# Performance work log

Measured on AMD Instinct MI355X. Metric: run time of the kernel, lower is better.

## Reference

```python
import jax, jax.numpy as jnp
import numpy as np

B = 4096
N_DENSE = 13
N_SPARSE = 26
VOCAB = 100000
EMB = 8
CIN_SIZE = [26, 128, 128]


def setup_inputs() -> dict:
    key = jax.random.key(0)
    ks = jax.random.split(key, 24)
    s = 0.05
    dense = jax.random.normal(ks[0], (B, N_DENSE), dtype=jnp.float32)
    sparse = jax.random.randint(ks[1], (B, N_SPARSE), 0, VOCAB).astype(jnp.float32)
    inputs = jnp.concatenate([dense, sparse], axis=1)  # [B, 39]
    emb_tables = jax.random.normal(ks[2], (N_SPARSE, VOCAB, EMB), dtype=jnp.float32) * s
    linear_W = jax.random.normal(ks[3], (39, 1), dtype=jnp.float32) * s
    linear_b = jnp.zeros((1,), dtype=jnp.float32)
    # CIN Conv3d weights: kernel (H_prev, H0, 1) with out_channels H_next -> [H_next, H_prev, H0]
    W_cin0 = jax.random.normal(ks[4], (CIN_SIZE[1], CIN_SIZE[0], CIN_SIZE[0]), dtype=jnp.float32) * s
    b_cin0 = jnp.zeros((CIN_SIZE[1],), dtype=jnp.float32)
    W_cin1 = jax.random.normal(ks[5], (CIN_SIZE[2], CIN_SIZE[1], CIN_SIZE[0]), dtype=jnp.float32) * s
    b_cin1 = jnp.zeros((CIN_SIZE[2],), dtype=jnp.float32)
    cin_lin_W = jax.random.normal(ks[6], (256, 1), dtype=jnp.float32) * s
    cin_lin_b = jnp.zeros((1,), dtype=jnp.float32)
    d_W1 = jax.random.normal(ks[7], (221, 256), dtype=jnp.float32) * s
    d_b1 = jnp.zeros((256,), dtype=jnp.float32)
    d_W2 = jax.random.normal(ks[8], (256, 128), dtype=jnp.float32) * s
    d_b2 = jnp.zeros((128,), dtype=jnp.float32)
    d_W3 = jax.random.normal(ks[9], (128, 64), dtype=jnp.float32) * s
    d_b3 = jnp.zeros((64,), dtype=jnp.float32)
    d_W4 = jax.random.normal(ks[10], (64, 1), dtype=jnp.float32) * s
    d_b4 = jnp.zeros((1,), dtype=jnp.float32)
    return dict(inputs=inputs, emb_tables=emb_tables, linear_W=linear_W, linear_b=linear_b,
                W_cin0=W_cin0, b_cin0=b_cin0, W_cin1=W_cin1, b_cin1=b_cin1,
                cin_lin_W=cin_lin_W, cin_lin_b=cin_lin_b,
                d_W1=d_W1, d_b1=d_b1, d_W2=d_W2, d_b2=d_b2,
                d_W3=d_W3, d_b3=d_b3, d_W4=d_W4, d_b4=d_b4)


def reference(inputs, emb_tables, linear_W, linear_b,
              W_cin0, b_cin0, W_cin1, b_cin1, cin_lin_W, cin_lin_b,
              d_W1, d_b1, d_W2, d_b2, d_W3, d_b3, d_W4, d_b4):
    dense_in = inputs[:, :N_DENSE]                       # [B, 13]
    sparse_idx = inputs[:, N_DENSE:].astype(jnp.int32)   # [B, 26]

    # linear part over the raw inputs
    linear_out = inputs @ linear_W + linear_b            # [B, 1]

    # per-field embedding lookup: tables [F, V, E], idx [B, F] -> emb [B, F, E]
    emb = jax.vmap(lambda t, i: t[i], in_axes=(0, 1), out_axes=1)(emb_tables, sparse_idx)

    # CIN: each layer is an outer product over fields followed by a full-extent
    # Conv3d, i.e. X_{l+1}[b,o,k] = sum_{i,j} X_l[b,i,k] * X_0[b,j,k] * W[o,i,j] + b[o]
    X0 = emb
    Xi = emb
    res = []
    for W, b in ((W_cin0, b_cin0), (W_cin1, b_cin1)):
        Xi = jnp.einsum('bik,bjk,oij->bok', Xi, X0, W) + b[None, :, None]
        res.append(Xi)
    cin_feat = jnp.sum(jnp.concatenate(res, axis=1), axis=-1)  # [B, 256]
    cin_out = jax.nn.relu(cin_feat @ cin_lin_W + cin_lin_b)    # [B, 1]

    # dense MLP over [dense | flattened embeddings]
    h = jnp.concatenate([dense_in, emb.reshape(emb.shape[0], -1)], axis=1)  # [B, 221]
    h = jax.nn.relu(h @ d_W1 + d_b1)
    h = jax.nn.relu(h @ d_W2 + d_b2)
    h = jax.nn.relu(h @ d_W3 + d_b3)
    dense_out = jax.nn.relu(h @ d_W4 + d_b4)                   # [B, 1]

    return jax.nn.sigmoid(linear_out + cin_out + dense_out).reshape(-1)  # [B]
```

## Files before the change

### kernel.cpp

```cpp
#include <hip/hip_runtime.h>
#include <math.h>

#define B     4096
#define ND    13
#define NS    26
#define NF    39
#define VOCAB 100000
#define NP    351
#define NPP   360
#define CHP   45
#define GSTR  28
#define RPB   4
#define XSS   212

#define OFF_GST 0
#define OFF_CST 10080
#define OFF_C2J 10088

__global__ __launch_bounds__(256) void k_pre(const float* __restrict__ W0,
                                             const float* __restrict__ W1,
                                             const float* __restrict__ b0,
                                             const float* __restrict__ b1,
                                             const float* __restrict__ clw,
                                             float* __restrict__ Gst,
                                             float* __restrict__ cst,
                                             float* __restrict__ c2j) {
    int blk = blockIdx.x, tid = threadIdx.x;
    if (blk < 26) {
        int j = blk;
        __shared__ float vh[2][128];
        __shared__ float vj[128];
        __shared__ float c2r[2];
        {
            int i = tid & 127, h = tid >> 7;
            const float* wp = W1 + (long)(h * 64) * 3328 + i * 26 + j;
            float acc = 0.f;
#pragma unroll 8
            for (int o = 0; o < 64; o++) acc += clw[128 + h * 64 + o] * wp[o * 3328];
            vh[h][i] = acc;
        }
        __syncthreads();
        if (tid < 128) {
            float vv = vh[0][tid] + vh[1][tid];
            vj[tid] = vv;
            float c = vv * b0[tid];
            for (int off = 32; off; off >>= 1) c += __shfl_down(c, off, 64);
            if ((tid & 63) == 0) c2r[tid >> 6] = c;
        }
        __syncthreads();
        if (tid == 0) c2j[j] = c2r[0] + c2r[1];
        for (int p = tid; p < NPP; p += 256) {
            float g = 0.f;
            if (p < NP) {
                int l = 0, rem = p;
                while (rem >= NS - l) { rem -= NS - l; l++; }
                int m = l + rem;
                float sym = (l != m) ? 1.f : 0.f;
                const float* wa = W0 + l * 26 + m;
                const float* wb = W0 + m * 26 + l;
#pragma unroll 8
                for (int i = 0; i < 128; i++)
                    g += vj[i] * (wa[i * 676] + sym * wb[i * 676]);
            }
            Gst[p * GSTR + j] = g;
        }
    } else if (blk == 26) {
        for (int p = tid; p < NPP; p += 256) {
            float a = 0.f; int lmbits = 0;
            if (p < NP) {
                int l = 0, rem = p;
                while (rem >= NS - l) { rem -= NS - l; l++; }
                int m = l + rem;
                float sym = (l != m) ? 1.f : 0.f;
                const float* wa = W0 + l * 26 + m;
                const float* wb = W0 + m * 26 + l;
#pragma unroll 8
                for (int o = 0; o < 128; o++)
                    a += clw[o] * (wa[o * 676] + sym * wb[o * 676]);
                lmbits = (l << 5) | m;
            }
            Gst[p * GSTR + 26] = a;
            Gst[p * GSTR + 27] = __int_as_float(lmbits);
        }
    } else {
        __shared__ float red[2];
        float c = 0.f;
        if (tid < 128) {
            c = clw[tid] * b0[tid] + clw[128 + tid] * b1[tid];
            for (int off = 32; off; off >>= 1) c += __shfl_down(c, off, 64);
            if ((tid & 63) == 0) red[tid >> 6] = c;
        }
        __syncthreads();
        if (tid == 0) cst[0] = 8.f * (red[0] + red[1]);
    }
}

__global__ __launch_bounds__(256, 4) void k_main(
    const float* __restrict__ inputs, const float* __restrict__ tables,
    const float* __restrict__ lW, const float* __restrict__ lb,
    const float* __restrict__ Gst, const float* __restrict__ c2j,
    const float* __restrict__ cst,
    const float* __restrict__ dW1, const float* __restrict__ db1,
    const float* __restrict__ dW2, const float* __restrict__ db2,
    const float* __restrict__ dW3, const float* __restrict__ db3,
    const float* __restrict__ dW4, const float* __restrict__ db4,
    const float* __restrict__ clb,
    float* __restrict__ out) {
    __shared__ float insf[RPB][40];
    __shared__ float xs[RPB][XSS];
    __shared__ float inT[256][RPB];
    __shared__ float h1T[256][RPB];
    __shared__ float h2T[128][RPB];
    __shared__ float lin_s[RPB], scin_s[RPB];
    __shared__ float redbuf[4][RPB];
    float* inF = &inT[0][0];

    int tid = threadIdx.x;
    int b0r = blockIdx.x * RPB;

    for (int t = tid; t < RPB * NF; t += 256) {
        int r = t / NF, c = t - r * NF;
        insf[r][c] = inputs[(b0r + r) * NF + c];
    }
    __syncthreads();

    if (tid < RPB * NS) {
        int r = tid / NS, f = tid - r * NS;
        int idx = (int)insf[r][ND + f];
        const float4* src = (const float4*)(tables + ((long)f * VOCAB + idx) * 8);
        float4 a = src[0], b4 = src[1];
        float4* dst = (float4*)&xs[r][f * 8];
        dst[0] = a; dst[1] = b4;
        int cb = ND + f * 8;
        inT[cb + 0][r] = a.x;  inT[cb + 1][r] = a.y;
        inT[cb + 2][r] = a.z;  inT[cb + 3][r] = a.w;
        inT[cb + 4][r] = b4.x; inT[cb + 5][r] = b4.y;
        inT[cb + 6][r] = b4.z; inT[cb + 7][r] = b4.w;
    }
    if (tid >= 128 && tid < 128 + RPB * ND) {
        int t = tid - 128;
        int r = t / ND, c = t - r * ND;
        inT[c][r] = insf[r][c];
    }
    if (tid >= 192 && tid < 192 + RPB) {
        int r = tid - 192;
        float acc = lb[0];
        for (int c = 0; c < NF; c++) acc += insf[r][c] * lW[c];
        lin_s[r] = acc;
    }
    __syncthreads();

    {
        int lane = tid & 63, w = tid >> 6;
        int pg = lane >> 5;
        int r = (lane >> 3) & 3;
        int k = lane & 7;
        int chunk = w * 2 + pg;
        const float* xrow = &xs[r][0];
        float t[27];
#pragma unroll
        for (int j = 0; j < 27; j++) t[j] = 0.f;
        const float4* grow = (const float4*)(Gst + chunk * CHP * GSTR);
#pragma unroll 2
        for (int pi = 0; pi < CHP; pi++) {
            float4 g6 = grow[pi * 7 + 6];
            int lm = __float_as_int(g6.w);
            float q = xrow[(lm >> 5) * 8 + k] * xrow[(lm & 31) * 8 + k];
            float4 g0 = grow[pi * 7 + 0], g1 = grow[pi * 7 + 1];
            float4 g2 = grow[pi * 7 + 2], g3 = grow[pi * 7 + 3];
            float4 g4 = grow[pi * 7 + 4], g5 = grow[pi * 7 + 5];
            t[0]  += g0.x * q; t[1]  += g0.y * q; t[2]  += g0.z * q; t[3]  += g0.w * q;
            t[4]  += g1.x * q; t[5]  += g1.y * q; t[6]  += g1.z * q; t[7]  += g1.w * q;
            t[8]  += g2.x * q; t[9]  += g2.y * q; t[10] += g2.z * q; t[11] += g2.w * q;
            t[12] += g3.x * q; t[13] += g3.y * q; t[14] += g3.z * q; t[15] += g3.w * q;
            t[16] += g4.x * q; t[17] += g4.y * q; t[18] += g4.z * q; t[19] += g4.w * q;
            t[20] += g5.x * q; t[21] += g5.y * q; t[22] += g5.z * q; t[23] += g5.w * q;
            t[24] += g6.x * q; t[25] += g6.y * q; t[26] += g6.z * q;
        }
        float csel = (chunk == 0) ? 1.f : 0.f;
        float part = t[26];
#pragma unroll
        for (int j = 0; j < 26; j++) {
            float xv = xrow[j * 8 + k];
            part += (t[j] + csel * c2j[j]) * xv;
        }
        part += __shfl_xor(part, 1, 64);
        part += __shfl_xor(part, 2, 64);
        part += __shfl_xor(part, 4, 64);
        part += __shfl_xor(part, 32, 64);
        if ((lane & 39) == 0) redbuf[w][r] = part;
    }
    __syncthreads();

    if (tid < RPB) {
        float s = cst[0];
        for (int w = 0; w < 4; w++) s += redbuf[w][tid];
        scin_s[tid] = s;
    }
    {
        float bias = db1[tid];
        float a0 = bias, a1 = bias, a2 = bias, a3 = bias;
        for (int c = 0; c < 221; c++) {
            float wv = dW1[c * 256 + tid];
            float4 iv = *(const float4*)&inT[c][0];
            a0 += iv.x * wv; a1 += iv.y * wv; a2 += iv.z * wv; a3 += iv.w * wv;
        }
        float4 o0;
        o0.x = fmaxf(a0, 0.f); o0.y = fmaxf(a1, 0.f);
        o0.z = fmaxf(a2, 0.f); o0.w = fmaxf(a3, 0.f);
        *(float4*)&h1T[tid][0] = o0;
    }
    __syncthreads();

    {
        int o = tid & 127, cg = tid >> 7;
        float bias = (cg == 0) ? db2[o] : 0.f;
        float a0 = bias, a1 = bias, a2 = bias, a3 = bias;
        const float* wbase = dW2 + cg * 128 * 128 + o;
        const float* hbase = &h1T[cg * 128][0];
        for (int c = 0; c < 128; c++) {
            float wv = wbase[c * 128];
            float4 iv = *(const float4*)(hbase + c * RPB);
            a0 += iv.x * wv; a1 += iv.y * wv; a2 += iv.z * wv; a3 += iv.w * wv;
        }
        *(float4*)&inF[tid * 4] = make_float4(a0, a1, a2, a3);
    }
    __syncthreads();
    if (tid < 128) {
        float4 p0 = *(const float4*)&inF[tid * 4];
        float4 p1 = *(const float4*)&inF[(tid + 128) * 4];
        float4 o0;
        o0.x = fmaxf(p0.x + p1.x, 0.f); o0.y = fmaxf(p0.y + p1.y, 0.f);
        o0.z = fmaxf(p0.z + p1.z, 0.f); o0.w = fmaxf(p0.w + p1.w, 0.f);
        *(float4*)&h2T[tid][0] = o0;
    }
    __syncthreads();

    {
        int o = tid & 63, cg = tid >> 6;
        float bias = (cg == 0) ? db3[o] : 0.f;
        float a0 = bias, a1 = bias, a2 = bias, a3 = bias;
        const float* wbase = dW3 + cg * 32 * 64 + o;
        const float* hbase = &h2T[cg * 32][0];
        for (int c = 0; c < 32; c++) {
            float wv = wbase[c * 64];
            float4 iv = *(const float4*)(hbase + c * RPB);
            a0 += iv.x * wv; a1 += iv.y * wv; a2 += iv.z * wv; a3 += iv.w * wv;
        }
        *(float4*)&inF[tid * 4] = make_float4(a0, a1, a2, a3);
    }
    __syncthreads();

    if (tid < 64) {
        float s0 = 0.f, s1 = 0.f, s2 = 0.f, s3 = 0.f;
#pragma unroll
        for (int cg = 0; cg < 4; cg++) {
            float4 pv = *(const float4*)&inF[(cg * 64 + tid) * 4];
            s0 += pv.x; s1 += pv.y; s2 += pv.z; s3 += pv.w;
        }
        float w4 = dW4[tid];
        s0 = fmaxf(s0, 0.f) * w4; s1 = fmaxf(s1, 0.f) * w4;
        s2 = fmaxf(s2, 0.f) * w4; s3 = fmaxf(s3, 0.f) * w4;
#pragma unroll
        for (int off = 1; off < 64; off <<= 1) {
            s0 += __shfl_xor(s0, off, 64);
            s1 += __shfl_xor(s1, off, 64);
            s2 += __shfl_xor(s2, off, 64);
            s3 += __shfl_xor(s3, off, 64);
        }
        if (tid == 0) {
            float sv[4] = { s0, s1, s2, s3 };
            float bb = db4[0], cb = clb[0];
#pragma unroll
            for (int r = 0; r < RPB; r++) {
                float dense = fmaxf(sv[r] + bb, 0.f);
                float cin = fmaxf(scin_s[r] + cb, 0.f);
                float x = lin_s[r] + cin + dense;
                out[b0r + r] = 1.f / (1.f + expf(-x));
            }
        }
    }
}

extern "C" void kernel_launch(void* const* d_in, const int* in_sizes, int n_in,
                              void* d_out, int out_size, void* d_ws, size_t ws_size,
                              hipStream_t stream) {
    const float* inputs = (const float*)d_in[0];
    const float* tables = (const float*)d_in[1];
    const float* lW     = (const float*)d_in[2];
    const float* lb     = (const float*)d_in[3];
    const float* W0     = (const float*)d_in[4];
    const float* b0     = (const float*)d_in[5];
    const float* W1c    = (const float*)d_in[6];
    const float* b1c    = (const float*)d_in[7];
    const float* clw    = (const float*)d_in[8];
    const float* clb    = (const float*)d_in[9];
    const float* dW1    = (const float*)d_in[10];
    const float* db1    = (const float*)d_in[11];
    const float* dW2    = (const float*)d_in[12];
    const float* db2    = (const float*)d_in[13];
    const float* dW3    = (const float*)d_in[14];
    const float* db3    = (const float*)d_in[15];
    const float* dW4    = (const float*)d_in[16];
    const float* db4    = (const float*)d_in[17];

    float* ws   = (float*)d_ws;
    float* Gst  = ws + OFF_GST;
    float* cst  = ws + OFF_CST;
    float* c2j  = ws + OFF_C2J;

    k_pre<<<28, 256, 0, stream>>>(W0, W1c, b0, b1c, clw, Gst, cst, c2j);
    k_main<<<B / RPB, 256, 0, stream>>>(inputs, tables, lW, lb, Gst, c2j, cst,
                                        dW1, db1, dW2, db2, dW3, db3, dW4, db4, clb,
                                        (float*)d_out);
}
```

Before: 227.1 us.

## Register-tile MLP layers 4x4 with float4 weight loads and split-K shared reduction

Each thread now computes a 4-output by 4-row tile using float4 weight loads and splits the input channel dimension across thread groups, with partial sums written to a new swizzled shared buffer and reduced afterwards. The transposed input staging for the first MLP layer moves after the embedding gather into a simple strided loop. The aim is fewer global weight loads per FMA and more instruction-level parallelism in the dense MLP. The cost is an extra 16KB of shared memory, which may reduce occupancy, plus additional reduction passes and barriers.

```diff
diff --git a/kernel.cpp b/kernel.cpp
--- a/kernel.cpp
+++ b/kernel.cpp
@@ -111,9 +111,9 @@
     __shared__ float inT[256][RPB];
     __shared__ float h1T[256][RPB];
     __shared__ float h2T[128][RPB];
+    __shared__ float4 pbuf4[1024];
     __shared__ float lin_s[RPB], scin_s[RPB];
     __shared__ float redbuf[4][RPB];
-    float* inF = &inT[0][0];
 
     int tid = threadIdx.x;
     int b0r = blockIdx.x * RPB;
@@ -131,16 +131,6 @@
         float4 a = src[0], b4 = src[1];
         float4* dst = (float4*)&xs[r][f * 8];
         dst[0] = a; dst[1] = b4;
-        int cb = ND + f * 8;
-        inT[cb + 0][r] = a.x;  inT[cb + 1][r] = a.y;
-        inT[cb + 2][r] = a.z;  inT[cb + 3][r] = a.w;
-        inT[cb + 4][r] = b4.x; inT[cb + 5][r] = b4.y;
-        inT[cb + 6][r] = b4.z; inT[cb + 7][r] = b4.w;
-    }
-    if (tid >= 128 && tid < 128 + RPB * ND) {
-        int t = tid - 128;
-        int r = t / ND, c = t - r * ND;
-        inT[c][r] = insf[r][c];
     }
     if (tid >= 192 && tid < 192 + RPB) {
         int r = tid - 192;
@@ -149,6 +139,11 @@
         lin_s[r] = acc;
     }
     __syncthreads();
+
+    for (int e = tid; e < 221 * RPB; e += 256) {
+        int c = e >> 2, r = e & 3;
+        inT[c][r] = (c < ND) ? insf[r][c] : xs[r][c - ND];
+    }
 
     {
         int lane = tid & 63, w = tid >> 6;
@@ -198,69 +193,124 @@
         scin_s[tid] = s;
     }
     {
-        float bias = db1[tid];
-        float a0 = bias, a1 = bias, a2 = bias, a3 = bias;
-        for (int c = 0; c < 221; c++) {
-            float wv = dW1[c * 256 + tid];
+        int oq = tid & 63, cg = tid >> 6;
+        int c0 = cg * 55 + (cg != 0);
+        int c1 = (cg + 1) * 55 + 1;
+        float4 a0 = make_float4(0.f, 0.f, 0.f, 0.f);
+        float4 a1 = make_float4(0.f, 0.f, 0.f, 0.f);
+        float4 a2 = make_float4(0.f, 0.f, 0.f, 0.f);
+        float4 a3 = make_float4(0.f, 0.f, 0.f, 0.f);
+#pragma unroll 4
+        for (int c = c0; c < c1; c++) {
+            float4 wv = *(const float4*)&dW1[c * 256 + (oq << 2)];
             float4 iv = *(const float4*)&inT[c][0];
-            a0 += iv.x * wv; a1 += iv.y * wv; a2 += iv.z * wv; a3 += iv.w * wv;
-        }
+            a0.x += iv.x * wv.x; a0.y += iv.y * wv.x; a0.z += iv.z * wv.x; a0.w += iv.w * wv.x;
+            a1.x += iv.x * wv.y; a1.y += iv.y * wv.y; a1.z += iv.z * wv.y; a1.w += iv.w * wv.y;
+            a2.x += iv.x * wv.z; a2.y += iv.y * wv.z; a2.z += iv.z * wv.z; a2.w += iv.w * wv.z;
+            a3.x += iv.x * wv.w; a3.y += iv.y * wv.w; a3.z += iv.z * wv.w; a3.w += iv.w * wv.w;
+        }
+        int pb = (cg << 8) + (oq << 2);
+        pbuf4[pb + ((0 + oq) & 3)] = a0;
+        pbuf4[pb + ((1 + oq) & 3)] = a1;
+        pbuf4[pb + ((2 + oq) & 3)] = a2;
+        pbuf4[pb + ((3 + oq) & 3)] = a3;
+    }
+    __syncthreads();
+    {
+        int oq = tid >> 2, j = tid & 3;
+        int base = (oq << 2) + ((j + oq) & 3);
+        float4 p0 = pbuf4[base];
+        float4 p1 = pbuf4[256 + base];
+        float4 p2 = pbuf4[512 + base];
+        float4 p3 = pbuf4[768 + base];
+        float bb = db1[tid];
         float4 o0;
-        o0.x = fmaxf(a0, 0.f); o0.y = fmaxf(a1, 0.f);
-        o0.z = fmaxf(a2, 0.f); o0.w = fmaxf(a3, 0.f);
+        o0.x = fmaxf(p0.x + p1.x + p2.x + p3.x + bb, 0.f);
+        o0.y = fmaxf(p0.y + p1.y + p2.y + p3.y + bb, 0.f);
+        o0.z = fmaxf(p0.z + p1.z + p2.z + p3.z + bb, 0.f);
+        o0.w = fmaxf(p0.w + p1.w + p2.w + p3.w + bb, 0.f);
         *(float4*)&h1T[tid][0] = o0;
     }
     __syncthreads();
 
     {
-        int o = tid & 127, cg = tid >> 7;
-        float bias = (cg == 0) ? db2[o] : 0.f;
-        float a0 = bias, a1 = bias, a2 = bias, a3 = bias;
-        const float* wbase = dW2 + cg * 128 * 128 + o;
-        const float* hbase = &h1T[cg * 128][0];
-        for (int c = 0; c < 128; c++) {
-            float wv = wbase[c * 128];
-            float4 iv = *(const float4*)(hbase + c * RPB);
-            a0 += iv.x * wv; a1 += iv.y * wv; a2 += iv.z * wv; a3 += iv.w * wv;
-        }
-        *(float4*)&inF[tid * 4] = make_float4(a0, a1, a2, a3);
+        int oq = tid & 31, cg = tid >> 5;
+        int c0 = cg << 5;
+        float4 a0 = make_float4(0.f, 0.f, 0.f, 0.f);
+        float4 a1 = make_float4(0.f, 0.f, 0.f, 0.f);
+        float4 a2 = make_float4(0.f, 0.f, 0.f, 0.f);
+        float4 a3 = make_float4(0.f, 0.f, 0.f, 0.f);
+#pragma unroll 4
+        for (int cc = 0; cc < 32; cc++) {
+            int c = c0 + cc;
+            float4 wv = *(const float4*)&dW2[c * 128 + (oq << 2)];
+            float4 iv = *(const float4*)&h1T[c][0];
+            a0.x += iv.x * wv.x; a0.y += iv.y * wv.x; a0.z += iv.z * wv.x; a0.w += iv.w * wv.x;
+            a1.x += iv.x * wv.y; a1.y += iv.y * wv.y; a1.z += iv.z * wv.y; a1.w += iv.w * wv.y;
+            a2.x += iv.x * wv.z; a2.y += iv.y * wv.z; a2.z += iv.z * wv.z; a2.w += iv.w * wv.z;
+            a3.x += iv.x * wv.w; a3.y += iv.y * wv.w; a3.z += iv.z * wv.w; a3.w += iv.w * wv.w;
+        }
+        int pb = (cg << 7) + (oq << 2);
+        pbuf4[pb + ((0 + oq) & 3)] = a0;
+        pbuf4[pb + ((1 + oq) & 3)] = a1;
+        pbuf4[pb + ((2 + oq) & 3)] = a2;
+        pbuf4[pb + ((3 + oq) & 3)] = a3;
     }
     __syncthreads();
     if (tid < 128) {
-        float4 p0 = *(const float4*)&inF[tid * 4];
-        float4 p1 = *(const float4*)&inF[(tid + 128) * 4];
+        int oq = tid >> 2, j = tid & 3;
+        int base = (oq << 2) + ((j + oq) & 3);
+        float sx = db2[tid], sy = sx, sz = sx, sw = sx;
+#pragma unroll
+        for (int cg = 0; cg < 8; cg++) {
+            float4 pv = pbuf4[(cg << 7) + base];
+            sx += pv.x; sy += pv.y; sz += pv.z; sw += pv.w;
+        }
         float4 o0;
-        o0.x = fmaxf(p0.x + p1.x, 0.f); o0.y = fmaxf(p0.y + p1.y, 0.f);
-        o0.z = fmaxf(p0.z + p1.z, 0.f); o0.w = fmaxf(p0.w + p1.w, 0.f);
+        o0.x = fmaxf(sx, 0.f); o0.y = fmaxf(sy, 0.f);
+        o0.z = fmaxf(sz, 0.f); o0.w = fmaxf(sw, 0.f);
         *(float4*)&h2T[tid][0] = o0;
     }
     __syncthreads();
 
     {
-        int o = tid & 63, cg = tid >> 6;
-        float bias = (cg == 0) ? db3[o] : 0.f;
-        float a0 = bias, a1 = bias, a2 = bias, a3 = bias;
-        const float* wbase = dW3 + cg * 32 * 64 + o;
-        const float* hbase = &h2T[cg * 32][0];
-        for (int c = 0; c < 32; c++) {
-            float wv = wbase[c * 64];
-            float4 iv = *(const float4*)(hbase + c * RPB);
-            a0 += iv.x * wv; a1 += iv.y * wv; a2 += iv.z * wv; a3 += iv.w * wv;
-        }
-        *(float4*)&inF[tid * 4] = make_float4(a0, a1, a2, a3);
+        int oq = tid & 15, cg = tid >> 4;
+        int c0 = cg << 3;
+        float4 a0 = make_float4(0.f, 0.f, 0.f, 0.f);
+        float4 a1 = make_float4(0.f, 0.f, 0.f, 0.f);
+        float4 a2 = make_float4(0.f, 0.f, 0.f, 0.f);
+        float4 a3 = make_float4(0.f, 0.f, 0.f, 0.f);
+#pragma unroll
+        for (int cc = 0; cc < 8; cc++) {
+            int c = c0 + cc;
+            float4 wv = *(const float4*)&dW3[c * 64 + (oq << 2)];
+            float4 iv = *(const float4*)&h2T[c][0];
+            a0.x += iv.x * wv.x; a0.y += iv.y * wv.x; a0.z += iv.z * wv.x; a0.w += iv.w * wv.x;
+            a1.x += iv.x * wv.y; a1.y += iv.y * wv.y; a1.z += iv.z * wv.y; a1.w += iv.w * wv.y;
+            a2.x += iv.x * wv.z; a2.y += iv.y * wv.z; a2.z += iv.z * wv.z; a2.w += iv.w * wv.z;
+            a3.x += iv.x * wv.w; a3.y += iv.y * wv.w; a3.z += iv.z * wv.w; a3.w += iv.w * wv.w;
+        }
+        int pb = (cg << 6) + (oq << 2);
+        pbuf4[pb + ((0 + oq) & 3)] = a0;
+        pbuf4[pb + ((1 + oq) & 3)] = a1;
+        pbuf4[pb + ((2 + oq) & 3)] = a2;
+        pbuf4[pb + ((3 + oq) & 3)] = a3;
     }
     __syncthreads();
 
     if (tid < 64) {
+        int oq = tid >> 2, j = tid & 3;
+        int base = (oq << 2) + ((j + oq) & 3);
         float s0 = 0.f, s1 = 0.f, s2 = 0.f, s3 = 0.f;
 #pragma unroll
-        for (int cg = 0; cg < 4; cg++) {
-            float4 pv = *(const float4*)&inF[(cg * 64 + tid) * 4];
+        for (int cg = 0; cg < 16; cg++) {
+            float4 pv = pbuf4[(cg << 6) + base];
             s0 += pv.x; s1 += pv.y; s2 += pv.z; s3 += pv.w;
         }
+        float b3 = db3[tid];
         float w4 = dW4[tid];
-        s0 = fmaxf(s0, 0.f) * w4; s1 = fmaxf(s1, 0.f) * w4;
-        s2 = fmaxf(s2, 0.f) * w4; s3 = fmaxf(s3, 0.f) * w4;
+        s0 = fmaxf(s0 + b3, 0.f) * w4; s1 = fmaxf(s1 + b3, 0.f) * w4;
+        s2 = fmaxf(s2 + b3, 0.f) * w4; s3 = fmaxf(s3 + b3, 0.f) * w4;
 #pragma unroll
         for (int off = 1; off < 64; off <<= 1) {
             s0 += __shfl_xor(s0, off, 64);
```

Result: no change. 226.8 us (-0.1%).

## Process 16 rows per 512-thread block with shared-memory CIN coefficients

Applied to the files above, without the earlier changes.

Raises rows per block from 4 to 16 and threads per block to 512, so each MLP weight loaded from global memory is reused across 16 batch rows instead of 4. The CIN coefficient table is staged into shared memory once per block, and each MLP layer's input-channel reduction is split across thread groups and combined through a swizzled shared buffer. The intent is to cut global weight traffic, at the cost of much larger shared memory per block, more registers, fewer blocks in the grid, and extra reduction passes and barriers.

```diff
diff --git a/kernel.cpp b/kernel.cpp
--- a/kernel.cpp
+++ b/kernel.cpp
@@ -10,7 +10,8 @@
 #define NPP   360
 #define CHP   45
 #define GSTR  28
-#define RPB   4
+#define RPB   16
+#define TPB   512
 #define XSS   212
 
 #define OFF_GST 0
@@ -95,7 +96,7 @@
     }
 }
 
-__global__ __launch_bounds__(256, 4) void k_main(
+__global__ __launch_bounds__(512, 2) void k_main(
     const float* __restrict__ inputs, const float* __restrict__ tables,
     const float* __restrict__ lW, const float* __restrict__ lb,
     const float* __restrict__ Gst, const float* __restrict__ c2j,
@@ -106,20 +107,24 @@
     const float* __restrict__ dW4, const float* __restrict__ db4,
     const float* __restrict__ clb,
     float* __restrict__ out) {
+    __shared__ float4 sGst4[NPP * 7];
     __shared__ float insf[RPB][40];
     __shared__ float xs[RPB][XSS];
-    __shared__ float inT[256][RPB];
+    __shared__ float inT[221][RPB];
     __shared__ float h1T[256][RPB];
     __shared__ float h2T[128][RPB];
+    __shared__ float4 pbuf4[2048];
     __shared__ float lin_s[RPB], scin_s[RPB];
-    __shared__ float redbuf[4][RPB];
-    float* inF = &inT[0][0];
+    __shared__ float redbuf[8][RPB];
+    __shared__ float c2s[26];
 
     int tid = threadIdx.x;
     int b0r = blockIdx.x * RPB;
 
-    for (int t = tid; t < RPB * NF; t += 256) {
-        int r = t / NF, c = t - r * NF;
+    for (int i = tid; i < NPP * 7; i += TPB) sGst4[i] = ((const float4*)Gst)[i];
+    if (tid < 26) c2s[tid] = c2j[tid];
+    for (int e = tid; e < RPB * NF; e += TPB) {
+        int r = e / NF, c = e - r * NF;
         insf[r][c] = inputs[(b0r + r) * NF + c];
     }
     __syncthreads();
@@ -131,145 +136,235 @@
         float4 a = src[0], b4 = src[1];
         float4* dst = (float4*)&xs[r][f * 8];
         dst[0] = a; dst[1] = b4;
-        int cb = ND + f * 8;
-        inT[cb + 0][r] = a.x;  inT[cb + 1][r] = a.y;
-        inT[cb + 2][r] = a.z;  inT[cb + 3][r] = a.w;
-        inT[cb + 4][r] = b4.x; inT[cb + 5][r] = b4.y;
-        inT[cb + 6][r] = b4.z; inT[cb + 7][r] = b4.w;
-    }
-    if (tid >= 128 && tid < 128 + RPB * ND) {
-        int t = tid - 128;
-        int r = t / ND, c = t - r * ND;
-        inT[c][r] = insf[r][c];
-    }
-    if (tid >= 192 && tid < 192 + RPB) {
-        int r = tid - 192;
+    }
+    if (tid >= 448 && tid < 448 + RPB) {
+        int r = tid - 448;
         float acc = lb[0];
         for (int c = 0; c < NF; c++) acc += insf[r][c] * lW[c];
         lin_s[r] = acc;
     }
     __syncthreads();
 
+    for (int e = tid; e < 221 * RPB; e += TPB) {
+        int c = e >> 4, r = e & 15;
+        inT[c][r] = (c < ND) ? insf[r][c] : xs[r][c - ND];
+    }
+
     {
         int lane = tid & 63, w = tid >> 6;
-        int pg = lane >> 5;
-        int r = (lane >> 3) & 3;
-        int k = lane & 7;
-        int chunk = w * 2 + pg;
-        const float* xrow = &xs[r][0];
-        float t[27];
-#pragma unroll
-        for (int j = 0; j < 27; j++) t[j] = 0.f;
-        const float4* grow = (const float4*)(Gst + chunk * CHP * GSTR);
+        int rlo = lane >> 3, k = lane & 7;
+        const float4* grow = &sGst4[w * CHP * 7];
+        float csel = (w == 0) ? 1.f : 0.f;
+#pragma unroll 1
+        for (int h = 0; h < 2; h++) {
+            int row = (h << 3) + rlo;
+            const float* xrow = &xs[row][0];
+            float t[27];
+#pragma unroll
+            for (int j = 0; j < 27; j++) t[j] = 0.f;
 #pragma unroll 2
-        for (int pi = 0; pi < CHP; pi++) {
-            float4 g6 = grow[pi * 7 + 6];
-            int lm = __float_as_int(g6.w);
-            float q = xrow[(lm >> 5) * 8 + k] * xrow[(lm & 31) * 8 + k];
-            float4 g0 = grow[pi * 7 + 0], g1 = grow[pi * 7 + 1];
-            float4 g2 = grow[pi * 7 + 2], g3 = grow[pi * 7 + 3];
-            float4 g4 = grow[pi * 7 + 4], g5 = grow[pi * 7 + 5];
-            t[0]  += g0.x * q; t[1]  += g0.y * q; t[2]  += g0.z * q; t[3]  += g0.w * q;
-            t[4]  += g1.x * q; t[5]  += g1.y * q; t[6]  += g1.z * q; t[7]  += g1.w * q;
-            t[8]  += g2.x * q; t[9]  += g2.y * q; t[10] += g2.z * q; t[11] += g2.w * q;
-            t[12] += g3.x * q; t[13] += g3.y * q; t[14] += g3.z * q; t[15] += g3.w * q;
-            t[16] += g4.x * q; t[17] += g4.y * q; t[18] += g4.z * q; t[19] += g4.w * q;
-            t[20] += g5.x * q; t[21] += g5.y * q; t[22] += g5.z * q; t[23] += g5.w * q;
-            t[24] += g6.x * q; t[25] += g6.y * q; t[26] += g6.z * q;
-        }
-        float csel = (chunk == 0) ? 1.f : 0.f;
-        float part = t[26];
-#pragma unroll
-        for (int j = 0; j < 26; j++) {
-            float xv = xrow[j * 8 + k];
-            part += (t[j] + csel * c2j[j]) * xv;
-        }
-        part += __shfl_xor(part, 1, 64);
-        part += __shfl_xor(part, 2, 64);
-        part += __shfl_xor(part, 4, 64);
-        part += __shfl_xor(part, 32, 64);
-        if ((lane & 39) == 0) redbuf[w][r] = part;
+            for (int pi = 0; pi < CHP; pi++) {
+                float4 g6 = grow[pi * 7 + 6];
+                int lm = __float_as_int(g6.w);
+                float q = xrow[(lm >> 5) * 8 + k] * xrow[(lm & 31) * 8 + k];
+                float4 g0 = grow[pi * 7 + 0], g1 = grow[pi * 7 + 1];
+                float4 g2 = grow[pi * 7 + 2], g3 = grow[pi * 7 + 3];
+                float4 g4 = grow[pi * 7 + 4], g5 = grow[pi * 7 + 5];
+                t[0]  += g0.x * q; t[1]  += g0.y * q; t[2]  += g0.z * q; t[3]  += g0.w * q;
+                t[4]  += g1.x * q; t[5]  += g1.y * q; t[6]  += g1.z * q; t[7]  += g1.w * q;
+                t[8]  += g2.x * q; t[9]  += g2.y * q; t[10] += g2.z * q; t[11] += g2.w * q;
+                t[12] += g3.x * q; t[13] += g3.y * q; t[14] += g3.z * q; t[15] += g3.w * q;
+                t[16] += g4.x * q; t[17] += g4.y * q; t[18] += g4.z * q; t[19] += g4.w * q;
+                t[20] += g5.x * q; t[21] += g5.y * q; t[22] += g5.z * q; t[23] += g5.w * q;
+                t[24] += g6.x * q; t[25] += g6.y * q; t[26] += g6.z * q;
+            }
+            float part = t[26];
+#pragma unroll
+            for (int j = 0; j < 26; j++) {
+                float xv = xrow[j * 8 + k];
+                part += (t[j] + csel * c2s[j]) * xv;
+            }
+            part += __shfl_xor(part, 1, 64);
+            part += __shfl_xor(part, 2, 64);
+            part += __shfl_xor(part, 4, 64);
+            if (k == 0) redbuf[w][row] = part;
+        }
     }
     __syncthreads();
 
     if (tid < RPB) {
         float s = cst[0];
-        for (int w = 0; w < 4; w++) s += redbuf[w][tid];
+#pragma unroll
+        for (int w = 0; w < 8; w++) s += redbuf[w][tid];
         scin_s[tid] = s;
     }
     {
-        float bias = db1[tid];
-        float a0 = bias, a1 = bias, a2 = bias, a3 = bias;
-        for (int c = 0; c < 221; c++) {
-            float wv = dW1[c * 256 + tid];
-            float4 iv = *(const float4*)&inT[c][0];
-            a0 += iv.x * wv; a1 += iv.y * wv; a2 += iv.z * wv; a3 += iv.w * wv;
-        }
-        float4 o0;
-        o0.x = fmaxf(a0, 0.f); o0.y = fmaxf(a1, 0.f);
-        o0.z = fmaxf(a2, 0.f); o0.w = fmaxf(a3, 0.f);
-        *(float4*)&h1T[tid][0] = o0;
+        int o = tid & 255, cg = tid >> 8;
+        int c0 = cg ? 111 : 0;
+        int c1 = cg ? 221 : 111;
+        float4 A0 = make_float4(0.f, 0.f, 0.f, 0.f);
+        float4 A1 = A0, A2 = A0, A3 = A0;
+#pragma unroll 4
+        for (int c = c0; c < c1; c++) {
+            float wv = dW1[c * 256 + o];
+            const float4* ivp = (const float4*)&inT[c][0];
+            float4 i0 = ivp[0], i1 = ivp[1], i2 = ivp[2], i3 = ivp[3];
+            A0.x += i0.x * wv; A0.y += i0.y * wv; A0.z += i0.z * wv; A0.w += i0.w * wv;
+            A1.x += i1.x * wv; A1.y += i1.y * wv; A1.z += i1.z * wv; A1.w += i1.w * wv;
+            A2.x += i2.x * wv; A2.y += i2.y * wv; A2.z += i2.z * wv; A2.w += i2.w * wv;
+            A3.x += i3.x * wv; A3.y += i3.y * wv; A3.z += i3.z * wv; A3.w += i3.w * wv;
+        }
+        int pb = (cg << 10) + (o << 2);
+        pbuf4[pb + ((0 + o) & 3)] = A0;
+        pbuf4[pb + ((1 + o) & 3)] = A1;
+        pbuf4[pb + ((2 + o) & 3)] = A2;
+        pbuf4[pb + ((3 + o) & 3)] = A3;
+    }
+    __syncthreads();
+    if (tid < 256) {
+        int o = tid, base = o << 2;
+        float bb = db1[o];
+        float4 S0, S1, S2, S3;
+        {
+            int s = (0 + o) & 3;
+            float4 p = pbuf4[base + s], q = pbuf4[1024 + base + s];
+            S0.x = fmaxf(p.x + q.x + bb, 0.f); S0.y = fmaxf(p.y + q.y + bb, 0.f);
+            S0.z = fmaxf(p.z + q.z + bb, 0.f); S0.w = fmaxf(p.w + q.w + bb, 0.f);
+        }
+        {
+            int s = (1 + o) & 3;
+            float4 p = pbuf4[base + s], q = pbuf4[1024 + base + s];
+            S1.x = fmaxf(p.x + q.x + bb, 0.f); S1.y = fmaxf(p.y + q.y + bb, 0.f);
+            S1.z = fmaxf(p.z + q.z + bb, 0.f); S1.w = fmaxf(p.w + q.w + bb, 0.f);
+        }
+        {
+            int s = (2 + o) & 3;
+            float4 p = pbuf4[base + s], q = pbuf4[1024 + base + s];
+            S2.x = fmaxf(p.x + q.x + bb, 0.f); S2.y = fmaxf(p.y + q.y + bb, 0.f);
+            S2.z = fmaxf(p.z + q.z + bb, 0.f); S2.w = fmaxf(p.w + q.w + bb, 0.f);
+        }
+        {
+            int s = (3 + o) & 3;
+            float4 p = pbuf4[base + s], q = pbuf4[1024 + base + s];
+            S3.x = fmaxf(p.x + q.x + bb, 0.f); S3.y = fmaxf(p.y + q.y + bb, 0.f);
+            S3.z = fmaxf(p.z + q.z + bb, 0.f); S3.w = fmaxf(p.w + q.w + bb, 0.f);
+        }
+        *(float4*)&h1T[o][0]  = S0;
+        *(float4*)&h1T[o][4]  = S1;
+        *(float4*)&h1T[o][8]  = S2;
+        *(float4*)&h1T[o][12] = S3;
     }
     __syncthreads();
 
     {
         int o = tid & 127, cg = tid >> 7;
-        float bias = (cg == 0) ? db2[o] : 0.f;
-        float a0 = bias, a1 = bias, a2 = bias, a3 = bias;
-        const float* wbase = dW2 + cg * 128 * 128 + o;
-        const float* hbase = &h1T[cg * 128][0];
-        for (int c = 0; c < 128; c++) {
-            float wv = wbase[c * 128];
-            float4 iv = *(const float4*)(hbase + c * RPB);
-            a0 += iv.x * wv; a1 += iv.y * wv; a2 += iv.z * wv; a3 += iv.w * wv;
-        }
-        *(float4*)&inF[tid * 4] = make_float4(a0, a1, a2, a3);
+        int c0 = cg << 6;
+        float4 A0 = make_float4(0.f, 0.f, 0.f, 0.f);
+        float4 A1 = A0, A2 = A0, A3 = A0;
+#pragma unroll 4
+        for (int cc = 0; cc < 64; cc++) {
+            int c = c0 + cc;
+            float wv = dW2[c * 128 + o];
+            const float4* ivp = (const float4*)&h1T[c][0];
+            float4 i0 = ivp[0], i1 = ivp[1], i2 = ivp[2], i3 = ivp[3];
+            A0.x += i0.x * wv; A0.y += i0.y * wv; A0.z += i0.z * wv; A0.w += i0.w * wv;
+            A1.x += i1.x * wv; A1.y += i1.y * wv; A1.z += i1.z * wv; A1.w += i1.w * wv;
+            A2.x += i2.x * wv; A2.y += i2.y * wv; A2.z += i2.z * wv; A2.w += i2.w * wv;
+            A3.x += i3.x * wv; A3.y += i3.y * wv; A3.z += i3.z * wv; A3.w += i3.w * wv;
+        }
+        int pb = (cg << 9) + (o << 2);
+        pbuf4[pb + ((0 + o) & 3)] = A0;
+        pbuf4[pb + ((1 + o) & 3)] = A1;
+        pbuf4[pb + ((2 + o) & 3)] = A2;
+        pbuf4[pb + ((3 + o) & 3)] = A3;
     }
     __syncthreads();
     if (tid < 128) {
-        float4 p0 = *(const float4*)&inF[tid * 4];
-        float4 p1 = *(const float4*)&inF[(tid + 128) * 4];
-        float4 o0;
-        o0.x = fmaxf(p0.x + p1.x, 0.f); o0.y = fmaxf(p0.y + p1.y, 0.f);
-        o0.z = fmaxf(p0.z + p1.z, 0.f); o0.w = fmaxf(p0.w + p1.w, 0.f);
-        *(float4*)&h2T[tid][0] = o0;
+        int o = tid, base = o << 2;
+        float bb = db2[o];
+        float4 S[4];
+#pragma unroll
+        for (int j = 0; j < 4; j++) {
+            int s = (j + o) & 3;
+            float sx = bb, sy = bb, sz = bb, sw = bb;
+#pragma unroll
+            for (int cg = 0; cg < 4; cg++) {
+                float4 pv = pbuf4[(cg << 9) + base + s];
+                sx += pv.x; sy += pv.y; sz += pv.z; sw += pv.w;
+            }
+            S[j].x = fmaxf(sx, 0.f); S[j].y = fmaxf(sy, 0.f);
+            S[j].z = fmaxf(sz, 0.f); S[j].w = fmaxf(sw, 0.f);
+        }
+        *(float4*)&h2T[o][0]  = S[0];
+        *(float4*)&h2T[o][4]  = S[1];
+        *(float4*)&h2T[o][8]  = S[2];
+        *(float4*)&h2T[o][12] = S[3];
     }
     __syncthreads();
 
     {
         int o = tid & 63, cg = tid >> 6;
-        float bias = (cg == 0) ? db3[o] : 0.f;
-        float a0 = bias, a1 = bias, a2 = bias, a3 = bias;
-        const float* wbase = dW3 + cg * 32 * 64 + o;
-        const float* hbase = &h2T[cg * 32][0];
-        for (int c = 0; c < 32; c++) {
-            float wv = wbase[c * 64];
-            float4 iv = *(const float4*)(hbase + c * RPB);
-            a0 += iv.x * wv; a1 += iv.y * wv; a2 += iv.z * wv; a3 += iv.w * wv;
-        }
-        *(float4*)&inF[tid * 4] = make_float4(a0, a1, a2, a3);
+        int c0 = cg << 4;
+        float4 A0 = make_float4(0.f, 0.f, 0.f, 0.f);
+        float4 A1 = A0, A2 = A0, A3 = A0;
+#pragma unroll
+        for (int cc = 0; cc < 16; cc++) {
+            int c = c0 + cc;
+            float wv = dW3[c * 64 + o];
+            const float4* ivp = (const float4*)&h2T[c][0];
+            float4 i0 = ivp[0], i1 = ivp[1], i2 = ivp[2], i3 = ivp[3];
+            A0.x += i0.x * wv; A0.y += i0.y * wv; A0.z += i0.z * wv; A0.w += i0.w * wv;
+            A1.x += i1.x * wv; A1.y += i1.y * wv; A1.z += i1.z * wv; A1.w += i1.w * wv;
+            A2.x += i2.x * wv; A2.y += i2.y * wv; A2.z += i2.z * wv; A2.w += i2.w * wv;
+            A3.x += i3.x * wv; A3.y += i3.y * wv; A3.z += i3.z * wv; A3.w += i3.w * wv;
+        }
+        int pb = (cg << 8) + (o << 2);
+        pbuf4[pb + ((0 + o) & 3)] = A0;
+        pbuf4[pb + ((1 + o) & 3)] = A1;
+        pbuf4[pb + ((2 + o) & 3)] = A2;
+        pbuf4[pb + ((3 + o) & 3)] = A3;
     }
     __syncthreads();
 
     if (tid < 64) {
-        float s0 = 0.f, s1 = 0.f, s2 = 0.f, s3 = 0.f;
-#pragma unroll
-        for (int cg = 0; cg < 4; cg++) {
-            float4 pv = *(const float4*)&inF[(cg * 64 + tid) * 4];
-            s0 += pv.x; s1 += pv.y; s2 += pv.z; s3 += pv.w;
-        }
-        float w4 = dW4[tid];
-        s0 = fmaxf(s0, 0.f) * w4; s1 = fmaxf(s1, 0.f) * w4;
-        s2 = fmaxf(s2, 0.f) * w4; s3 = fmaxf(s3, 0.f) * w4;
+        int o = tid, base = o << 2;
+        float4 S0 = make_float4(0.f, 0.f, 0.f, 0.f);
+        float4 S1 = S0, S2 = S0, S3 = S0;
+#pragma unroll
+        for (int cg = 0; cg < 8; cg++) {
+            int pb = (cg << 8) + base;
+            float4 p0 = pbuf4[pb + ((0 + o) & 3)];
+            float4 p1 = pbuf4[pb + ((1 + o) & 3)];
+            float4 p2 = pbuf4[pb + ((2 + o) & 3)];
+            float4 p3 = pbuf4[pb + ((3 + o) & 3)];
+            S0.x += p0.x; S0.y += p0.y; S0.z += p0.z; S0.w += p0.w;
+            S1.x += p1.x; S1.y += p1.y; S1.z += p1.z; S1.w += p1.w;
+            S2.x += p2.x; S2.y += p2.y; S2.z += p2.z; S2.w += p2.w;
+            S3.x += p3.x; S3.y += p3.y; S3.z += p3.z; S3.w += p3.w;
+        }
+        float b3 = db3[o], w4 = dW4[o];
+        S0.x = fmaxf(S0.x + b3, 0.f) * w4; S0.y = fmaxf(S0.y + b3, 0.f) * w4;
+        S0.z = fmaxf(S0.z + b3, 0.f) * w4; S0.w = fmaxf(S0.w + b3, 0.f) * w4;
+        S1.x = fmaxf(S1.x + b3, 0.f) * w4; S1.y = fmaxf(S1.y + b3, 0.f) * w4;
+        S1.z = fmaxf(S1.z + b3, 0.f) * w4; S1.w = fmaxf(S1.w + b3, 0.f) * w4;
+        S2.x = fmaxf(S2.x + b3, 0.f) * w4; S2.y = fmaxf(S2.y + b3, 0.f) * w4;
+        S2.z = fmaxf(S2.z + b3, 0.f) * w4; S2.w = fmaxf(S2.w + b3, 0.f) * w4;
+        S3.x = fmaxf(S3.x + b3, 0.f) * w4; S3.y = fmaxf(S3.y + b3, 0.f) * w4;
+        S3.z = fmaxf(S3.z + b3, 0.f) * w4; S3.w = fmaxf(S3.w + b3, 0.f) * w4;
 #pragma unroll
         for (int off = 1; off < 64; off <<= 1) {
-            s0 += __shfl_xor(s0, off, 64);
-            s1 += __shfl_xor(s1, off, 64);
-            s2 += __shfl_xor(s2, off, 64);
-            s3 += __shfl_xor(s3, off, 64);
+            S0.x += __shfl_xor(S0.x, off, 64); S0.y += __shfl_xor(S0.y, off, 64);
+            S0.z += __shfl_xor(S0.z, off, 64); S0.w += __shfl_xor(S0.w, off, 64);
+            S1.x += __shfl_xor(S1.x, off, 64); S1.y += __shfl_xor(S1.y, off, 64);
+            S1.z += __shfl_xor(S1.z, off, 64); S1.w += __shfl_xor(S1.w, off, 64);
+            S2.x += __shfl_xor(S2.x, off, 64); S2.y += __shfl_xor(S2.y, off, 64);
+            S2.z += __shfl_xor(S2.z, off, 64); S2.w += __shfl_xor(S2.w, off, 64);
+            S3.x += __shfl_xor(S3.x, off, 64); S3.y += __shfl_xor(S3.y, off, 64);
+            S3.z += __shfl_xor(S3.z, off, 64); S3.w += __shfl_xor(S3.w, off, 64);
         }
         if (tid == 0) {
-            float sv[4] = { s0, s1, s2, s3 };
+            float sv[16] = { S0.x, S0.y, S0.z, S0.w, S1.x, S1.y, S1.z, S1.w,
+                             S2.x, S2.y, S2.z, S2.w, S3.x, S3.y, S3.z, S3.w };
             float bb = db4[0], cb = clb[0];
 #pragma unroll
             for (int r = 0; r < RPB; r++) {
@@ -310,7 +405,7 @@
     float* c2j  = ws + OFF_C2J;
 
     k_pre<<<28, 256, 0, stream>>>(W0, W1c, b0, b1c, clw, Gst, cst, c2j);
-    k_main<<<B / RPB, 256, 0, stream>>>(inputs, tables, lW, lb, Gst, c2j, cst,
+    k_main<<<B / RPB, TPB, 0, stream>>>(inputs, tables, lW, lb, Gst, c2j, cst,
                                         dW1, db1, dW2, db2, dW3, db3, dW4, db4, clb,
                                         (float*)d_out);
 }
```

Result: faster. 214.7 us (-5.4%).
